# Performance work log

Hardware: AMD Instinct MI355X
Metric: run time of the kernel (lower is better)

Reference implementation:

```python
import jax, jax.numpy as jnp
import numpy as np

STRIDE = (2, 2)
PADDING = (1, 1)
DILATION = (1, 1)
KERNEL = (3, 3)


def _out_hw(h_in, w_in):
    h_out = (h_in + 2 * PADDING[0] - DILATION[0] * (KERNEL[0] - 1) - 1) // STRIDE[0] + 1
    w_out = (w_in + 2 * PADDING[1] - DILATION[1] * (KERNEL[1] - 1) - 1) // STRIDE[1] + 1
    return h_out, w_out


def _stride_permutation(h_out, w_out):
    # Single-shot multiplexing row permutation (mirrors _get_stride_permutation).
    s_h, s_w = STRIDE
    if s_h == 1 and s_w == 1:
        return np.arange(h_out * w_out)
    perm = []
    for si in range(s_h):
        for sj in range(s_w):
            for i in range((h_out + s_h - 1) // s_h):
                ai = i * s_h + si
                if ai >= h_out:
                    continue
                for j in range((w_out + s_w - 1) // s_w):
                    aj = j * s_w + sj
                    if aj >= w_out:
                        continue
                    perm.append(ai * w_out + aj)
    return np.asarray(perm, dtype=np.int32)


def setup_inputs() -> dict:
    key = jax.random.key(0)
    kx, kw, kb = jax.random.split(key, 3)
    x = jax.random.normal(kx, (16, 256, 64, 64), dtype=jnp.float32)
    weight = jax.random.normal(kw, (256, 256, 3, 3), dtype=jnp.float32)
    bias = jax.random.normal(kb, (256,), dtype=jnp.float32)
    return {"x": x, "weight": weight, "bias": bias}


def reference(x, weight, bias):
    # Toeplitz matrix-vector product == grouped strided conv.
    out = jax.lax.conv_general_dilated(
        x, weight,
        window_strides=STRIDE,
        padding=[(PADDING[0], PADDING[0]), (PADDING[1], PADDING[1])],
        rhs_dilation=DILATION,
        dimension_numbers=("NCHW", "OIHW", "NCHW"),
        feature_group_count=1,
    )  # [B, Cout, h_out, w_out]
    b, c, h_out, w_out = out.shape
    perm = jnp.asarray(_stride_permutation(h_out, w_out))
    flat = out.reshape(b, c, h_out * w_out)
    # permuted[new_idx] = flat[perm[new_idx]] (single-shot stride multiplexing)
    permuted = flat[:, :, perm]
    return permuted + bias[None, :, None]
```

## Files before the change

### kernel.cpp

```cpp
#include <hip/hip_runtime.h>
#include <cstdint>

typedef __attribute__((ext_vector_type(8))) __bf16 bf16x8;
typedef __attribute__((ext_vector_type(4))) float f32x4;
typedef __attribute__((ext_vector_type(4))) uint32_t u32x4;

#define NB   16
#define CIN  256
#define COUT 256
#define HP   66
#define WP   66
#define KTOT 2304
#define XPB  (HP*WP*256)
#define XPAD_ELEMS (NB*XPB)

__device__ __forceinline__ uint16_t f2bf(float f) {
  uint32_t u = __builtin_bit_cast(uint32_t, f);
  u = (u + 0x7FFFu + ((u >> 16) & 1u)) >> 16;
  return (uint16_t)u;
}

__global__ void prep_kernel(const float* __restrict__ x, const float* __restrict__ w,
                            uint16_t* __restrict__ xpad, uint16_t* __restrict__ bw) {
  const int bid = blockIdx.x;
  const int tid = threadIdx.x;
  if (bid < 2048) {
    const int lane = tid & 63;
    const int wvi = tid >> 6;
    const int chalf = bid & 1;
    const int h = (bid >> 1) & 63;
    const int b = bid >> 7;
    const int cg = lane >> 4;
    const int w4 = (lane & 15) * 4;
    const int c0 = chalf * 128 + wvi * 32 + cg * 8;
    const float* src = x + ((size_t)(b * 256 + c0) * 64 + h) * 64 + w4;
    f32x4 v[8];
    #pragma unroll
    for (int j = 0; j < 8; ++j)
      v[j] = *(const f32x4*)(src + (size_t)j * 4096);
    uint16_t* dst = xpad + ((size_t)(b * HP + h + 1) * WP + 1 + w4) * 256 + c0;
    #pragma unroll
    for (int p = 0; p < 4; ++p) {
      u32x4 d;
      #pragma unroll
      for (int k = 0; k < 4; ++k)
        d[k] = (uint32_t)f2bf(v[2 * k][p]) | ((uint32_t)f2bf(v[2 * k + 1][p]) << 16);
      *(u32x4*)(dst + p * 256) = d;
    }
  } else if (bid < 3088) {
    const int idx = (bid - 2048) * 256 + tid;
    const int b = idx / 16640;
    const int r = idx - b * 16640;
    uint64_t* base = (uint64_t*)(xpad + (size_t)b * XPB);
    int off;
    if (r < 4224) {
      off = r;
    } else if (r < 8448) {
      off = 274560 + (r - 4224);
    } else if (r < 12544) {
      const int i = r - 8448;
      off = (1 + (i >> 6)) * 4224 + (i & 63);
    } else {
      const int i = r - 12544;
      off = (1 + (i >> 6)) * 4224 + 4160 + (i & 63);
    }
    base[off] = 0;
  } else {
    const int gid = (bid - 3088) * 256 + tid;
    const int co = gid / 288;
    const int r = gid - co * 288;
    const int tap = r >> 5;
    const int ci0 = (r & 31) * 8;
    u32x4 d;
    #pragma unroll
    for (int k = 0; k < 4; ++k) {
      const float v0 = w[((co * 256 + ci0 + 2 * k + 0) * 9) + tap];
      const float v1 = w[((co * 256 + ci0 + 2 * k + 1) * 9) + tap];
      d[k] = (uint32_t)f2bf(v0) | ((uint32_t)f2bf(v1) << 16);
    }
    *(u32x4*)(bw + co * KTOT + tap * 256 + ci0) = d;
  }
}

__device__ __forceinline__ void gl_lds16(const void* g, void* l) {
  __builtin_amdgcn_global_load_lds(
      (__attribute__((address_space(1))) void*)(uintptr_t)g,
      (__attribute__((address_space(3))) void*)(uint32_t)(uintptr_t)l,
      16, 0, 0);
}

__global__ __launch_bounds__(256, 1) void gemm_kernel(
    const uint16_t* __restrict__ xpad, const uint16_t* __restrict__ bw,
    const float* __restrict__ bias, float* __restrict__ out) {
  __shared__ uint16_t lA[3][128 * 64];
  __shared__ uint16_t lB[3][128 * 64];
  const int tid = threadIdx.x;
  const int wv = tid >> 6, lane = tid & 63;
  const int quad = lane >> 4, l15 = lane & 15, l7 = lane & 7;
  const int wm = wv >> 1, wn = wv & 1;

  const int xcd = blockIdx.x & 7;
  const int grp = blockIdx.x >> 3;
  const int mtile = (xcd << 4) + (grp >> 1);
  const int ntile = grp & 1;
  const int n0 = ntile * 128;
  const int m0 = mtile * 128;
  const int bidx = m0 >> 10;
  const int q0 = m0 & 1023;

  int a_goff[4];
  #pragma unroll
  for (int t = 0; t < 4; ++t) {
    const int slot = t * 256 + tid;
    const int row = slot >> 3;
    const int kc = (slot & 7) ^ (row & 7);
    const int p = q0 + row;
    const int oh = 2 * ((p >> 4) & 15) + ((p >> 9) & 1);
    const int ow = 2 * (p & 15) + ((p >> 8) & 1);
    a_goff[t] = ((bidx * HP + 2 * oh) * WP + 2 * ow) * 256 + kc * 8;
  }
  int b_goff[4];
  #pragma unroll
  for (int t = 0; t < 4; ++t) {
    const int slot = t * 256 + tid;
    const int n = slot >> 3;
    const int kc = (slot & 7) ^ (n & 7);
    b_goff[t] = (n0 + n) * KTOT + kc * 8;
  }

  int aoff[4][2], boff[4][2];
  #pragma unroll
  for (int r = 0; r < 4; ++r)
    #pragma unroll
    for (int s = 0; s < 2; ++s)
      aoff[r][s] = (wm * 64 + r * 16 + l15) * 128 + (((s * 4 + quad) ^ l7) * 16);
  #pragma unroll
  for (int c = 0; c < 4; ++c)
    #pragma unroll
    for (int s = 0; s < 2; ++s)
      boff[c][s] = (wn * 64 + c * 16 + l15) * 128 + (((s * 4 + quad) ^ l7) * 16);

  f32x4 acc[4][4];
  #pragma unroll
  for (int r = 0; r < 4; ++r)
    #pragma unroll
    for (int c = 0; c < 4; ++c)
      acc[r][c] = (f32x4){0.f, 0.f, 0.f, 0.f};

  auto stage = [&](int it, int buf) {
    const int tap = it >> 2;
    const int kh = tap / 3, kw = tap - kh * 3;
    const int ci0 = (it & 3) << 6;
    const uint16_t* aptr = xpad + (kh * WP + kw) * 256 + ci0;
    const uint16_t* bptr = bw + tap * 256 + ci0;
    char* la_ = (char*)&lA[buf][0];
    char* lb_ = (char*)&lB[buf][0];
    #pragma unroll
    for (int t = 0; t < 4; ++t)
      gl_lds16(aptr + a_goff[t], la_ + (t * 256 + wv * 64) * 16);
    #pragma unroll
    for (int t = 0; t < 4; ++t)
      gl_lds16(bptr + b_goff[t], lb_ + (t * 256 + wv * 64) * 16);
  };

  auto compute = [&](int buf) {
    const char* la = (const char*)&lA[buf][0];
    const char* lb = (const char*)&lB[buf][0];
    #pragma unroll
    for (int s = 0; s < 2; ++s) {
      bf16x8 af[4], bfr[4];
      #pragma unroll
      for (int r = 0; r < 4; ++r) af[r] = *(const bf16x8*)(la + aoff[r][s]);
      #pragma unroll
      for (int c = 0; c < 4; ++c) bfr[c] = *(const bf16x8*)(lb + boff[c][s]);
      #pragma unroll
      for (int r = 0; r < 4; ++r)
        #pragma unroll
        for (int c = 0; c < 4; ++c)
          acc[r][c] = __builtin_amdgcn_mfma_f32_16x16x32_bf16(af[r], bfr[c], acc[r][c], 0, 0, 0);
    }
  };

  stage(0, 0);
  stage(1, 1);
  int bcur = 0;
  for (int it = 0; it < 35; ++it) {
    asm volatile("s_waitcnt vmcnt(8)" ::: "memory");
    __builtin_amdgcn_s_barrier();
    asm volatile("" ::: "memory");
    if (it < 34) {
      int bnext = bcur + 2; if (bnext >= 3) bnext -= 3;
      stage(it + 2, bnext);
    }
    compute(bcur);
    bcur = (bcur == 2) ? 0 : bcur + 1;
  }
  asm volatile("s_waitcnt vmcnt(0)" ::: "memory");
  __builtin_amdgcn_s_barrier();
  asm volatile("" ::: "memory");
  compute(bcur);

  float* obase = out + (size_t)bidx * (COUT * 1024);
  #pragma unroll
  for (int c = 0; c < 4; ++c) {
    const int co = n0 + wn * 64 + c * 16 + l15;
    const float bv = bias[co];
    #pragma unroll
    for (int r = 0; r < 4; ++r) {
      const int q = q0 + wm * 64 + r * 16 + quad * 4;
      f32x4 v = acc[r][c];
      v += bv;
      *(f32x4*)(obase + (size_t)co * 1024 + q) = v;
    }
  }
}

extern "C" void kernel_launch(void* const* d_in, const int* in_sizes, int n_in,
                              void* d_out, int out_size, void* d_ws, size_t ws_size,
                              hipStream_t stream) {
  const float* x    = (const float*)d_in[0];
  const float* w    = (const float*)d_in[1];
  const float* bias = (const float*)d_in[2];
  float* out = (float*)d_out;
  uint16_t* xpad = (uint16_t*)d_ws;
  uint16_t* bwq  = xpad + XPAD_ELEMS;

  prep_kernel<<<dim3(3376), dim3(256), 0, stream>>>(x, w, xpad, bwq);
  gemm_kernel<<<dim3(256), dim3(256), 0, stream>>>(xpad, bwq, bias, out);
}
```

Measured before the change: 137.9 us.

## Load B fragments directly into registers and double-buffer only A in LDS

Weight fragments now go straight from global memory into per-wave register double buffers instead of through LDS, and LDS holds only a two-stage A buffer instead of three stages of A and B. The goal is to cut LDS traffic and footprint and drop the B LDS reads. In exchange, waves that share columns each fetch the same B data from global memory. The loads are 64-byte row fragments with a large stride. Using full __syncthreads instead of partial vmcnt waits also reduces load/compute overlap to one stage.

```diff
diff --git a/kernel.cpp b/kernel.cpp
--- a/kernel.cpp
+++ b/kernel.cpp
@@ -92,8 +92,7 @@
 __global__ __launch_bounds__(256, 1) void gemm_kernel(
     const uint16_t* __restrict__ xpad, const uint16_t* __restrict__ bw,
     const float* __restrict__ bias, float* __restrict__ out) {
-  __shared__ uint16_t lA[3][128 * 64];
-  __shared__ uint16_t lB[3][128 * 64];
+  __shared__ uint16_t lA[2][128 * 64];
   const int tid = threadIdx.x;
   const int wv = tid >> 6, lane = tid & 63;
   const int quad = lane >> 4, l15 = lane & 15, l7 = lane & 7;
@@ -119,26 +118,18 @@
     const int ow = 2 * (p & 15) + ((p >> 8) & 1);
     a_goff[t] = ((bidx * HP + 2 * oh) * WP + 2 * ow) * 256 + kc * 8;
   }
-  int b_goff[4];
-  #pragma unroll
-  for (int t = 0; t < 4; ++t) {
-    const int slot = t * 256 + tid;
-    const int n = slot >> 3;
-    const int kc = (slot & 7) ^ (n & 7);
-    b_goff[t] = (n0 + n) * KTOT + kc * 8;
-  }
-
-  int aoff[4][2], boff[4][2];
+
+  const uint16_t* bcolp[4];
+  #pragma unroll
+  for (int c = 0; c < 4; ++c)
+    bcolp[c] = bw + (size_t)(n0 + wn * 64 + c * 16 + l15) * KTOT + quad * 8;
+
+  int aoff[4][2];
   #pragma unroll
   for (int r = 0; r < 4; ++r)
     #pragma unroll
     for (int s = 0; s < 2; ++s)
       aoff[r][s] = (wm * 64 + r * 16 + l15) * 128 + (((s * 4 + quad) ^ l7) * 16);
-  #pragma unroll
-  for (int c = 0; c < 4; ++c)
-    #pragma unroll
-    for (int s = 0; s < 2; ++s)
-      boff[c][s] = (wn * 64 + c * 16 + l15) * 128 + (((s * 4 + quad) ^ l7) * 16);
 
   f32x4 acc[4][4];
   #pragma unroll
@@ -147,58 +138,69 @@
     for (int c = 0; c < 4; ++c)
       acc[r][c] = (f32x4){0.f, 0.f, 0.f, 0.f};
 
-  auto stage = [&](int it, int buf) {
+  auto stageA = [&](int it, int buf) {
     const int tap = it >> 2;
     const int kh = tap / 3, kw = tap - kh * 3;
     const int ci0 = (it & 3) << 6;
     const uint16_t* aptr = xpad + (kh * WP + kw) * 256 + ci0;
-    const uint16_t* bptr = bw + tap * 256 + ci0;
     char* la_ = (char*)&lA[buf][0];
-    char* lb_ = (char*)&lB[buf][0];
     #pragma unroll
     for (int t = 0; t < 4; ++t)
       gl_lds16(aptr + a_goff[t], la_ + (t * 256 + wv * 64) * 16);
-    #pragma unroll
-    for (int t = 0; t < 4; ++t)
-      gl_lds16(bptr + b_goff[t], lb_ + (t * 256 + wv * 64) * 16);
   };
 
-  auto compute = [&](int buf) {
+  auto loadB = [&](int it, bf16x8* dst) {
+    const int tap = it >> 2;
+    const int koff = tap * 256 + ((it & 3) << 6);
+    #pragma unroll
+    for (int c = 0; c < 4; ++c)
+      #pragma unroll
+      for (int s = 0; s < 2; ++s)
+        dst[c * 2 + s] = *(const bf16x8*)(bcolp[c] + koff + s * 32);
+  };
+
+  auto compute = [&](int buf, const bf16x8* bcur) {
     const char* la = (const char*)&lA[buf][0];
-    const char* lb = (const char*)&lB[buf][0];
     #pragma unroll
     for (int s = 0; s < 2; ++s) {
-      bf16x8 af[4], bfr[4];
+      bf16x8 af[4];
       #pragma unroll
       for (int r = 0; r < 4; ++r) af[r] = *(const bf16x8*)(la + aoff[r][s]);
-      #pragma unroll
-      for (int c = 0; c < 4; ++c) bfr[c] = *(const bf16x8*)(lb + boff[c][s]);
       #pragma unroll
       for (int r = 0; r < 4; ++r)
         #pragma unroll
         for (int c = 0; c < 4; ++c)
-          acc[r][c] = __builtin_amdgcn_mfma_f32_16x16x32_bf16(af[r], bfr[c], acc[r][c], 0, 0, 0);
+          acc[r][c] = __builtin_amdgcn_mfma_f32_16x16x32_bf16(af[r], bcur[c * 2 + s], acc[r][c], 0, 0, 0);
     }
   };
 
-  stage(0, 0);
-  stage(1, 1);
-  int bcur = 0;
-  for (int it = 0; it < 35; ++it) {
-    asm volatile("s_waitcnt vmcnt(8)" ::: "memory");
-    __builtin_amdgcn_s_barrier();
-    asm volatile("" ::: "memory");
-    if (it < 34) {
-      int bnext = bcur + 2; if (bnext >= 3) bnext -= 3;
-      stage(it + 2, bnext);
-    }
-    compute(bcur);
-    bcur = (bcur == 2) ? 0 : bcur + 1;
-  }
-  asm volatile("s_waitcnt vmcnt(0)" ::: "memory");
-  __builtin_amdgcn_s_barrier();
-  asm volatile("" ::: "memory");
-  compute(bcur);
+  bf16x8 bregA[8], bregB[8];
+
+  stageA(0, 0);
+  loadB(0, bregA);
+
+  for (int ih = 0; ih < 17; ++ih) {
+    {
+      const int it = 2 * ih;
+      __syncthreads();
+      stageA(it + 1, 1);
+      loadB(it + 1, bregB);
+      compute(0, bregA);
+    }
+    {
+      const int it = 2 * ih + 1;
+      __syncthreads();
+      stageA(it + 1, 0);
+      loadB(it + 1, bregA);
+      compute(1, bregB);
+    }
+  }
+  __syncthreads();
+  stageA(35, 1);
+  loadB(35, bregB);
+  compute(0, bregA);
+  __syncthreads();
+  compute(1, bregB);
 
   float* obase = out + (size_t)bidx * (COUT * 1024);
   #pragma unroll
```

New measurement: 162.9 us. 18.1% more time.
